# Kernel tuning notes

Measured on AMD Instinct MI355X. Metric: run time of the kernel, lower is better.

## Reference

```python
import jax, jax.numpy as jnp
import numpy as np

B, O, I, D = 8, 128, 128, 1024


def setup_inputs() -> dict:
    key = jax.random.key(0)
    ks = jax.random.split(key, 10)
    s = 1.0 / np.sqrt(2 * D)  # torch Linear default-ish scale
    return {
        "output": jax.random.normal(ks[0], (B, O, D), jnp.float32),
        "context": jax.random.normal(ks[1], (B, I, D), jnp.float32),
        "mask": jax.random.randint(ks[2], (B, I), 0, 2, jnp.int32),
        # self.w = Linear(2*dim, dim), split into the output-half and context-half
        "w_out_w": jax.random.normal(ks[3], (D, D), jnp.float32) * s,
        "w_ctx_w": jax.random.normal(ks[4], (D, D), jnp.float32) * s,
        "w_b": jax.random.normal(ks[5], (D,), jnp.float32) * s,
        # self.score = Linear(dim, 1)
        "score_w": jax.random.normal(ks[6], (D,), jnp.float32) * (1.0 / np.sqrt(D)),
        "score_b": jnp.zeros((), jnp.float32),
        # self.linear_out = Linear(2*dim, dim)
        "lin_w": jax.random.normal(ks[7], (2 * D, D), jnp.float32) * s,
        "lin_b": jax.random.normal(ks[8], (D,), jnp.float32) * s,
    }


def reference(output, context, mask, w_out_w, w_ctx_w, w_b, score_w, score_b, lin_w, lin_b):
    # Additive (Bahdanau) attention.
    # cat(out, ctx) @ W^T == out @ W1 + ctx @ W2  -> avoid [B,O,I,2D] concat.
    s_out = jnp.einsum('bod,de->boe', output, w_out_w)            # [B,O,D]
    s_ctx = jnp.einsum('bid,de->bie', context, w_ctx_w)           # [B,I,D]
    h = jax.nn.leaky_relu(s_out[:, :, None, :] + s_ctx[:, None, :, :] + w_b)  # [B,O,I,D]
    score = jnp.einsum('boid,d->boi', h, score_w) + score_b       # [B,O,I]
    score = jnp.where(mask[:, None, :] == 1, -jnp.inf, score)
    attn = jax.nn.softmax(score, axis=-1)                         # [B,O,I]
    attn_output = jnp.einsum('boi,bid->bod', attn, context)       # mix=True: bmm
    # fn=True: linear_out on cat(attn_output, output) then leaky_relu
    combined = jnp.concatenate([attn_output, output], axis=-1)    # [B,O,2D]
    attn_output = jax.nn.leaky_relu(combined @ lin_w + lin_b)     # [B,O,D]
    return attn_output, attn
```

## Files before the change

### kernel.cpp

```cpp
#include <hip/hip_runtime.h>

namespace {

constexpr int kB = 8, kO = 128, kI = 128, kD = 1024;
constexpr long kOutAttnOff = (long)kB * kO * kD;

typedef __attribute__((ext_vector_type(8))) short short8;
typedef __attribute__((ext_vector_type(4))) float f32x4;

__device__ __forceinline__ float leaky(float x) { return fmaxf(x, 0.01f * x); }

__device__ __forceinline__ short f2bf(float f) {
    unsigned u = __builtin_bit_cast(unsigned, f);
    u += 0x7FFFu + ((u >> 16) & 1u);
    return (short)(u >> 16);
}

__device__ __forceinline__ void gll16(const void* g, void* l) {
    __builtin_amdgcn_global_load_lds(
        (const __attribute__((address_space(1))) int*)g,
        (__attribute__((address_space(3))) int*)l, 16, 0, 0);
}

__global__ __launch_bounds__(256)
void conv_all(const float* __restrict__ output, const float* __restrict__ context,
              const float* __restrict__ w1, const float* __restrict__ w2,
              const float* __restrict__ lin,
              short* __restrict__ ob16, short* __restrict__ cb16,
              short* __restrict__ w1t, short* __restrict__ w2t,
              short* __restrict__ lint)
{
    __shared__ float T[64][68];
    const int bid = blockIdx.x, tid = threadIdx.x;

    if (bid < 1024) {
        const int idx = bid * 256 + tid;
        const float* src; short* dst; int i;
        if (idx < (1 << 17)) { src = output;  dst = ob16; i = idx; }
        else                 { src = context; dst = cb16; i = idx - (1 << 17); }
        const float4* s4 = (const float4*)src + (long)i * 2;
        const float4 v0 = s4[0], v1 = s4[1];
        short8 r;
        r[0] = f2bf(v0.x); r[1] = f2bf(v0.y); r[2] = f2bf(v0.z); r[3] = f2bf(v0.w);
        r[4] = f2bf(v1.x); r[5] = f2bf(v1.y); r[6] = f2bf(v1.z); r[7] = f2bf(v1.w);
        *(short8*)(dst + (long)i * 8) = r;
        return;
    }

    const int tb = bid - 1024;
    const float* src; short* dst; long C, R; int t2;
    if (tb < 256)      { src = w1;  dst = w1t;  R = 1024; C = 1024; t2 = tb; }
    else if (tb < 512) { src = w2;  dst = w2t;  R = 1024; C = 1024; t2 = tb - 256; }
    else               { src = lin; dst = lint; R = 2048; C = 1024; t2 = tb - 512; }
    const int tr = t2 >> 4, tc = t2 & 15;
    const int r = tid >> 2, q = tid & 3;

    const float* s = src + (long)(tr * 64 + r) * C + tc * 64 + q * 16;
    const float4 a0 = ((const float4*)s)[0];
    const float4 a1 = ((const float4*)s)[1];
    const float4 a2 = ((const float4*)s)[2];
    const float4 a3 = ((const float4*)s)[3];
    *(float4*)&T[r][q * 16 + 0]  = a0;
    *(float4*)&T[r][q * 16 + 4]  = a1;
    *(float4*)&T[r][q * 16 + 8]  = a2;
    *(float4*)&T[r][q * 16 + 12] = a3;
    __syncthreads();

    short8 o0, o1;
#pragma unroll
    for (int j = 0; j < 8; ++j)  o0[j] = f2bf(T[q * 16 + j][r]);
#pragma unroll
    for (int j = 0; j < 8; ++j)  o1[j] = f2bf(T[q * 16 + 8 + j][r]);
    short* dp = dst + (long)(tc * 64 + r) * R + tr * 64 + q * 16;
    *(short8*)dp       = o0;
    *((short8*)dp + 1) = o1;
}

__global__ __launch_bounds__(256)
void mm_jobs(const short* __restrict__ ob16, const short* __restrict__ cb16,
             const short* __restrict__ w1t, const short* __restrict__ w2t,
             const short* __restrict__ lint,
             const float* __restrict__ w_b, const float* __restrict__ lin_b,
             float* __restrict__ s_out, float* __restrict__ s_ctx,
             float* __restrict__ outlin, short* __restrict__ ctxlin)
{
    __shared__ short As[2][64][64];
    __shared__ short Bs[2][128][64];
    const int tid = threadIdx.x;
    const int t = blockIdx.x;
    const int lane = tid & 63, w = tid >> 6;

    const short *Ap, *Bp;
    int lda, ldb, bm, bn, ldc;
    const float* bias = nullptr;
    float* Cf = nullptr;
    short* Ch = nullptr;

    if (t < 384) {
        const int job = t >> 7, jt = t & 127;
        bm = (jt >> 3) * 64; bn = (jt & 7) * 128;
        lda = 1024; ldc = 1024;
        if (job == 0)      { Ap = ob16; Bp = w1t;         ldb = 1024; bias = w_b;   Cf = s_out;  }
        else if (job == 1) { Ap = cb16; Bp = w2t;         ldb = 1024;               Cf = s_ctx;  }
        else               { Ap = ob16; Bp = lint + 1024; ldb = 2048; bias = lin_b; Cf = outlin; }
    } else {
        const int tt = t - 384, bz = tt >> 4, tw = tt & 15;
        bm = tw * 64; bn = 0;
        Ap = lint; lda = 2048;
        Bp = cb16 + (long)bz * (kI * kD); ldb = 1024;
        Ch = ctxlin + (long)bz * (kD * kI); ldc = 128;
    }

    const int m0 = (w >> 1) * 32, n0 = (w & 1) * 64;
    const int fr = lane & 15, fcol = lane >> 4, sl = lane & 7;
    const int r8 = lane >> 3;
    const int sw8 = ((lane & 7) ^ r8) * 8;
    const int w16 = w * 16, w32 = w * 32;

    f32x4 acc[2][4] = {};

    auto stage = [&](int buf, int k0) {
        const short* ga = Ap + (long)(bm + w16 + r8) * lda + k0 + sw8;
        gll16(ga,                 &As[buf][w16][0]);
        gll16(ga + 8 * (long)lda, &As[buf][w16 + 8][0]);
        const short* gb = Bp + (long)(bn + w32 + r8) * ldb + k0 + sw8;
        gll16(gb,                  &Bs[buf][w32][0]);
        gll16(gb + 8 * (long)ldb,  &Bs[buf][w32 + 8][0]);
        gll16(gb + 16 * (long)ldb, &Bs[buf][w32 + 16][0]);
        gll16(gb + 24 * (long)ldb, &Bs[buf][w32 + 24][0]);
    };

    stage(0, 0);
    __syncthreads();
    int cur = 0;
    for (int s = 0; s < 16; ++s) {
        if (s < 15) stage(cur ^ 1, (s + 1) << 6);
#pragma unroll
        for (int ks8 = 0; ks8 < 8; ks8 += 4) {
            const int sa = ((ks8 + fcol) ^ sl) * 8;
            short8 a[2], b[4];
#pragma unroll
            for (int mi = 0; mi < 2; ++mi)
                a[mi] = *(const short8*)&As[cur][m0 + mi * 16 + fr][sa];
#pragma unroll
            for (int ni = 0; ni < 4; ++ni)
                b[ni] = *(const short8*)&Bs[cur][n0 + ni * 16 + fr][sa];
#pragma unroll
            for (int mi = 0; mi < 2; ++mi)
#pragma unroll
                for (int ni = 0; ni < 4; ++ni)
                    acc[mi][ni] = __builtin_amdgcn_mfma_f32_16x16x32_bf16(
                        a[mi], b[ni], acc[mi][ni], 0, 0, 0);
        }
        __syncthreads();
        cur ^= 1;
    }

    float bv[4] = {0, 0, 0, 0};
    if (bias) {
#pragma unroll
        for (int ni = 0; ni < 4; ++ni) bv[ni] = bias[bn + n0 + ni * 16 + fr];
    }
#pragma unroll
    for (int mi = 0; mi < 2; ++mi)
#pragma unroll
        for (int ni = 0; ni < 4; ++ni)
#pragma unroll
            for (int r = 0; r < 4; ++r) {
                const int row = bm + m0 + mi * 16 + ((lane >> 4) << 2) + r;
                const int col = bn + n0 + ni * 16 + fr;
                float v = acc[mi][ni][r] + bv[ni];
                if (Ch) Ch[(long)row * ldc + col] = f2bf(v);
                else    Cf[(long)row * ldc + col] = v;
            }
}

__global__ __launch_bounds__(256)
void score_softmax5(const float* __restrict__ s_out, const float* __restrict__ s_ctx,
                    const float* __restrict__ score_w, const float* __restrict__ score_b,
                    const int* __restrict__ mask, float* __restrict__ attn_f32,
                    short* __restrict__ attn_b16)
{
    __shared__ float As[4][1032];
    __shared__ float Cs[2][128][64];
    __shared__ float Wsh[1024];
    __shared__ float Ps[4][4][128];
    __shared__ int   Msk[128];

    const int b   = blockIdx.x;
    const int o0  = blockIdx.y * 4;
    const int tid = threadIdx.x;
    const int wv  = tid >> 6;
    const int ln  = tid & 63;

    const float* arow = s_out + (long)(b * kO + o0) * kD;
#pragma unroll
    for (int q = 0; q < 4; ++q) {
        const int tq = tid + q * 256;
        const int rr = tq >> 8, c4 = (tq & 255) * 4;
        *(float4*)&As[rr][c4] = *(const float4*)&arow[(long)rr * kD + c4];
    }
    *(float4*)&Wsh[tid * 4] = *(const float4*)&score_w[tid * 4];
    if (tid < 128) Msk[tid] = mask[b * kI + tid];

    const float* crow = s_ctx + (long)b * kI * kD;
    const int srow = wv * 4 + (ln >> 4);
    const int cho  = ((ln & 15) ^ (srow & 7)) * 4;

    auto stageCs = [&](int buf, int dc) {
#pragma unroll
        for (int it = 0; it < 8; ++it)
            gll16(crow + (long)(srow + it * 16) * kD + dc + cho,
                  &Cs[buf][wv * 4 + it * 16][0]);
    };

    float a0[4] = {}, a1[4] = {};
    const int kb = wv * 16;

    stageCs(0, 0);
    __syncthreads();
    int buf = 0;
    for (int c = 0; c < 16; ++c) {
        const int dc = c * 64;
        if (c < 15) stageCs(buf ^ 1, dc + 64);
#pragma unroll
        for (int kq = 0; kq < 4; ++kq) {
            const int sc = ((wv * 4 + kq) ^ (ln & 7)) * 4;
            const float4 c0 = *(const float4*)&Cs[buf][ln][sc];
            const float4 c1 = *(const float4*)&Cs[buf][ln + 64][sc];
            const float4 w4 = *(const float4*)&Wsh[dc + kb + kq * 4];
#pragma unroll
            for (int o = 0; o < 4; ++o) {
                const float4 av = *(const float4*)&As[o][dc + kb + kq * 4];
                a0[o] = fmaf(leaky(av.x + c0.x), w4.x, a0[o]);
                a0[o] = fmaf(leaky(av.y + c0.y), w4.y, a0[o]);
                a0[o] = fmaf(leaky(av.z + c0.z), w4.z, a0[o]);
                a0[o] = fmaf(leaky(av.w + c0.w), w4.w, a0[o]);
                a1[o] = fmaf(leaky(av.x + c1.x), w4.x, a1[o]);
                a1[o] = fmaf(leaky(av.y + c1.y), w4.y, a1[o]);
                a1[o] = fmaf(leaky(av.z + c1.z), w4.z, a1[o]);
                a1[o] = fmaf(leaky(av.w + c1.w), w4.w, a1[o]);
            }
        }
        __syncthreads();
        buf ^= 1;
    }

#pragma unroll
    for (int o = 0; o < 4; ++o) {
        Ps[wv][o][ln]      = a0[o];
        Ps[wv][o][ln + 64] = a1[o];
    }
    __syncthreads();

    const int ow = wv;
    const float negInf = -__builtin_huge_valf();
    const float sb = score_b[0];
    float s0 = Ps[0][ow][ln]      + Ps[1][ow][ln]
             + Ps[2][ow][ln]      + Ps[3][ow][ln]      + sb;
    float s1 = Ps[0][ow][ln + 64] + Ps[1][ow][ln + 64]
             + Ps[2][ow][ln + 64] + Ps[3][ow][ln + 64] + sb;
    if (Msk[ln]      != 0) s0 = negInf;
    if (Msk[ln + 64] != 0) s1 = negInf;

    float m = fmaxf(s0, s1);
#pragma unroll
    for (int d = 1; d < 64; d <<= 1) m = fmaxf(m, __shfl_xor(m, d, 64));
    const float e0 = __expf(s0 - m);
    const float e1 = __expf(s1 - m);
    float sum = e0 + e1;
#pragma unroll
    for (int d = 1; d < 64; d <<= 1) sum += __shfl_xor(sum, d, 64);
    const float inv = 1.0f / sum;

    const long rowoff = (long)(b * kO + o0 + ow) * kI;
    float* ro = attn_f32 + rowoff;
    short* rh = attn_b16 + rowoff;
    const float p0 = e0 * inv, p1 = e1 * inv;
    ro[ln]      = p0;
    ro[ln + 64] = p1;
    rh[ln]      = f2bf(p0);
    rh[ln + 64] = f2bf(p1);
}

__global__ __launch_bounds__(256)
void gemm_final(const short* __restrict__ A, const short* __restrict__ Bt,
                const float* __restrict__ addend, float* __restrict__ C)
{
    __shared__ short As[2][64][64];
    __shared__ short Bs[2][64][64];
    const int tid = threadIdx.x;
    const int bn = blockIdx.x * 64, bm = blockIdx.y * 64;
    const long z = blockIdx.z;
    const short* Az = A + z * (long)(kO * kI);
    const short* Bz = Bt + z * (long)(kD * kI);
    const float* adz = addend + z * (long)(kO * kD);
    float* Cz = C + z * (long)(kO * kD);

    const int lane = tid & 63, w = tid >> 6;
    const int w16 = w * 16;
    const int m0 = (w >> 1) * 32, n0 = (w & 1) * 32;
    const int fr = lane & 15, fcol = lane >> 4, sl = lane & 7;
    const int r8 = lane >> 3;
    const int sw8 = ((lane & 7) ^ r8) * 8;

    f32x4 acc[2][2] = {};

    auto stage = [&](int buf, int k0) {
        const short* ga = Az + (long)(bm + w16 + r8) * kI + k0 + sw8;
        gll16(ga,          &As[buf][w16][0]);
        gll16(ga + 8 * kI, &As[buf][w16 + 8][0]);
        const short* gb = Bz + (long)(bn + w16 + r8) * kI + k0 + sw8;
        gll16(gb,          &Bs[buf][w16][0]);
        gll16(gb + 8 * kI, &Bs[buf][w16 + 8][0]);
    };

    stage(0, 0);
    __syncthreads();
    int cur = 0;
    for (int s = 0; s < 2; ++s) {
        if (s == 0) stage(1, 64);
#pragma unroll
        for (int ks8 = 0; ks8 < 8; ks8 += 4) {
            const int sa = ((ks8 + fcol) ^ sl) * 8;
            const short8 a0 = *(const short8*)&As[cur][m0 + fr][sa];
            const short8 a1 = *(const short8*)&As[cur][m0 + 16 + fr][sa];
            const short8 b0 = *(const short8*)&Bs[cur][n0 + fr][sa];
            const short8 b1 = *(const short8*)&Bs[cur][n0 + 16 + fr][sa];
            acc[0][0] = __builtin_amdgcn_mfma_f32_16x16x32_bf16(a0, b0, acc[0][0], 0, 0, 0);
            acc[0][1] = __builtin_amdgcn_mfma_f32_16x16x32_bf16(a0, b1, acc[0][1], 0, 0, 0);
            acc[1][0] = __builtin_amdgcn_mfma_f32_16x16x32_bf16(a1, b0, acc[1][0], 0, 0, 0);
            acc[1][1] = __builtin_amdgcn_mfma_f32_16x16x32_bf16(a1, b1, acc[1][1], 0, 0, 0);
        }
        __syncthreads();
        cur ^= 1;
    }

#pragma unroll
    for (int mi = 0; mi < 2; ++mi)
#pragma unroll
        for (int ni = 0; ni < 2; ++ni)
#pragma unroll
            for (int r = 0; r < 4; ++r) {
                const int row = bm + m0 + mi * 16 + ((lane >> 4) << 2) + r;
                const int col = bn + n0 + ni * 16 + fr;
                const float v = acc[mi][ni][r] + adz[(long)row * kD + col];
                Cz[(long)row * kD + col] = leaky(v);
            }
}

}

extern "C" void kernel_launch(void* const* d_in, const int* in_sizes, int n_in,
                              void* d_out, int out_size, void* d_ws, size_t ws_size,
                              hipStream_t stream)
{
    const float* output  = (const float*)d_in[0];
    const float* context = (const float*)d_in[1];
    const int*   mask    = (const int*)d_in[2];
    const float* w_out_w = (const float*)d_in[3];
    const float* w_ctx_w = (const float*)d_in[4];
    const float* w_b     = (const float*)d_in[5];
    const float* score_w = (const float*)d_in[6];
    const float* score_b = (const float*)d_in[7];
    const float* lin_w   = (const float*)d_in[8];
    const float* lin_b   = (const float*)d_in[9];

    float* out_main = (float*)d_out;
    float* out_attn = out_main + kOutAttnOff;
    float* s_out    = out_main;

    char* wp = (char*)d_ws;
    float* s_ctx  = (float*)wp;  wp += (size_t)4 << 20;
    short* ob16   = (short*)wp;  wp += (size_t)2 << 20;
    short* cb16   = (short*)wp;  wp += (size_t)2 << 20;
    short* w1t    = (short*)wp;  wp += (size_t)2 << 20;
    short* w2t    = (short*)wp;  wp += (size_t)2 << 20;
    short* lint   = (short*)wp;  wp += (size_t)4 << 20;
    float* outlin = (float*)wp;  wp += (size_t)4 << 20;
    short* ctxlin = (short*)wp;  wp += (size_t)2 << 20;
    short* attn16 = (short*)wp;

    const dim3 blk(256);

    hipLaunchKernelGGL(conv_all, dim3(2048), blk, 0, stream,
        output, context, w_out_w, w_ctx_w, lin_w, ob16, cb16, w1t, w2t, lint);

    hipLaunchKernelGGL(mm_jobs, dim3(512), blk, 0, stream,
        ob16, cb16, w1t, w2t, lint, w_b, lin_b, s_out, s_ctx, outlin, ctxlin);

    hipLaunchKernelGGL(score_softmax5, dim3(8, 32), blk, 0, stream,
        s_out, s_ctx, score_w, score_b, mask, out_attn, attn16);

    hipLaunchKernelGGL(gemm_final, dim3(16, 2, 8), blk, 0, stream,
        attn16, ctxlin, outlin, out_main);
}
```

Measured before the change: 68.55 us.

## Fuse score softmax with final attention GEMM and rewrite leaky ReLU via abs

Merges the score/softmax kernel and the final attn·ctx GEMM into one kernel. Softmax probabilities stay in LDS as bf16 and feed MFMA tiles directly, which drops a launch and the bf16 attention round trip through global memory. Leaky ReLU is rewritten exactly as 0.505x + 0.495|x|. The linear part is split into a per-row output dot product and a per-column context dot product computed once, so the hot inner loop becomes add plus FMA with an abs modifier. In exchange, each block re-reads its batch's full ctxlin matrix and runs 16-row MFMAs with only 4 useful rows.

Result: slower. 72.30 us (+5.5%).

```diff
diff --git a/kernel.cpp b/kernel.cpp
--- a/kernel.cpp
+++ b/kernel.cpp
@@ -176,22 +176,28 @@
 }
 
 __global__ __launch_bounds__(256)
-void score_softmax5(const float* __restrict__ s_out, const float* __restrict__ s_ctx,
-                    const float* __restrict__ score_w, const float* __restrict__ score_b,
-                    const int* __restrict__ mask, float* __restrict__ attn_f32,
-                    short* __restrict__ attn_b16)
+void score_final(const float* __restrict__ s_out, const float* __restrict__ s_ctx,
+                 const float* __restrict__ score_w, const float* __restrict__ score_b,
+                 const int* __restrict__ mask, const short* __restrict__ ctxlin,
+                 const float* __restrict__ outlin, float* __restrict__ out_main,
+                 float* __restrict__ attn_f32)
 {
     __shared__ float As[4][1032];
-    __shared__ float Cs[2][128][64];
+    __shared__ __align__(16) char CsPool[65536];
     __shared__ float Wsh[1024];
     __shared__ float Ps[4][4][128];
+    __shared__ float Psi[4][128];
+    __shared__ float so_sh[4];
     __shared__ int   Msk[128];
-
+    __shared__ short Pl[16][136];
+
+    float (*Cs)[128][64] = reinterpret_cast<float(*)[128][64]>(CsPool);
     const int b   = blockIdx.x;
     const int o0  = blockIdx.y * 4;
     const int tid = threadIdx.x;
     const int wv  = tid >> 6;
     const int ln  = tid & 63;
+    const int fr  = ln & 15;
 
     const float* arow = s_out + (long)(b * kO + o0) * kD;
 #pragma unroll
@@ -202,6 +208,10 @@
     }
     *(float4*)&Wsh[tid * 4] = *(const float4*)&score_w[tid * 4];
     if (tid < 128) Msk[tid] = mask[b * kI + tid];
+    {
+        short* pf = &Pl[0][0];
+        for (int j = tid; j < 272; j += 256) *(short8*)(pf + j * 8) = short8{};
+    }
 
     const float* crow = s_ctx + (long)b * kI * kD;
     const int srow = wv * 4 + (ln >> 4);
@@ -214,11 +224,27 @@
                   &Cs[buf][wv * 4 + it * 16][0]);
     };
 
-    float a0[4] = {}, a1[4] = {};
-    const int kb = wv * 16;
-
     stageCs(0, 0);
     __syncthreads();
+
+    {
+        float acc = 0.0f;
+#pragma unroll
+        for (int j = 0; j < 16; j += 4) {
+            const float4 av = *(const float4*)&As[wv][ln * 16 + j];
+            const float4 ww = *(const float4*)&Wsh[ln * 16 + j];
+            acc = fmaf(av.x, ww.x, acc); acc = fmaf(av.y, ww.y, acc);
+            acc = fmaf(av.z, ww.z, acc); acc = fmaf(av.w, ww.w, acc);
+        }
+#pragma unroll
+        for (int d = 1; d < 64; d <<= 1) acc += __shfl_xor(acc, d, 64);
+        if (ln == 0) so_sh[wv] = acc;
+    }
+
+    float sa0[4] = {}, sa1[4] = {};
+    float si0 = 0.0f, si1 = 0.0f;
+    const int kb = wv * 16;
+
     int buf = 0;
     for (int c = 0; c < 16; ++c) {
         const int dc = c * 64;
@@ -229,17 +255,21 @@
             const float4 c0 = *(const float4*)&Cs[buf][ln][sc];
             const float4 c1 = *(const float4*)&Cs[buf][ln + 64][sc];
             const float4 w4 = *(const float4*)&Wsh[dc + kb + kq * 4];
+            si0 = fmaf(c0.x, w4.x, si0); si0 = fmaf(c0.y, w4.y, si0);
+            si0 = fmaf(c0.z, w4.z, si0); si0 = fmaf(c0.w, w4.w, si0);
+            si1 = fmaf(c1.x, w4.x, si1); si1 = fmaf(c1.y, w4.y, si1);
+            si1 = fmaf(c1.z, w4.z, si1); si1 = fmaf(c1.w, w4.w, si1);
 #pragma unroll
             for (int o = 0; o < 4; ++o) {
                 const float4 av = *(const float4*)&As[o][dc + kb + kq * 4];
-                a0[o] = fmaf(leaky(av.x + c0.x), w4.x, a0[o]);
-                a0[o] = fmaf(leaky(av.y + c0.y), w4.y, a0[o]);
-                a0[o] = fmaf(leaky(av.z + c0.z), w4.z, a0[o]);
-                a0[o] = fmaf(leaky(av.w + c0.w), w4.w, a0[o]);
-                a1[o] = fmaf(leaky(av.x + c1.x), w4.x, a1[o]);
-                a1[o] = fmaf(leaky(av.y + c1.y), w4.y, a1[o]);
-                a1[o] = fmaf(leaky(av.z + c1.z), w4.z, a1[o]);
-                a1[o] = fmaf(leaky(av.w + c1.w), w4.w, a1[o]);
+                sa0[o] = fmaf(__builtin_fabsf(av.x + c0.x), w4.x, sa0[o]);
+                sa0[o] = fmaf(__builtin_fabsf(av.y + c0.y), w4.y, sa0[o]);
+                sa0[o] = fmaf(__builtin_fabsf(av.z + c0.z), w4.z, sa0[o]);
+                sa0[o] = fmaf(__builtin_fabsf(av.w + c0.w), w4.w, sa0[o]);
+                sa1[o] = fmaf(__builtin_fabsf(av.x + c1.x), w4.x, sa1[o]);
+                sa1[o] = fmaf(__builtin_fabsf(av.y + c1.y), w4.y, sa1[o]);
+                sa1[o] = fmaf(__builtin_fabsf(av.z + c1.z), w4.z, sa1[o]);
+                sa1[o] = fmaf(__builtin_fabsf(av.w + c1.w), w4.w, sa1[o]);
             }
         }
         __syncthreads();
@@ -248,105 +278,95 @@
 
 #pragma unroll
     for (int o = 0; o < 4; ++o) {
-        Ps[wv][o][ln]      = a0[o];
-        Ps[wv][o][ln + 64] = a1[o];
-    }
+        Ps[wv][o][ln]      = sa0[o];
+        Ps[wv][o][ln + 64] = sa1[o];
+    }
+    Psi[wv][ln]      = si0;
+    Psi[wv][ln + 64] = si1;
     __syncthreads();
 
-    const int ow = wv;
-    const float negInf = -__builtin_huge_valf();
-    const float sb = score_b[0];
-    float s0 = Ps[0][ow][ln]      + Ps[1][ow][ln]
-             + Ps[2][ow][ln]      + Ps[3][ow][ln]      + sb;
-    float s1 = Ps[0][ow][ln + 64] + Ps[1][ow][ln + 64]
-             + Ps[2][ow][ln + 64] + Ps[3][ow][ln + 64] + sb;
-    if (Msk[ln]      != 0) s0 = negInf;
-    if (Msk[ln + 64] != 0) s1 = negInf;
-
-    float m = fmaxf(s0, s1);
-#pragma unroll
-    for (int d = 1; d < 64; d <<= 1) m = fmaxf(m, __shfl_xor(m, d, 64));
-    const float e0 = __expf(s0 - m);
-    const float e1 = __expf(s1 - m);
-    float sum = e0 + e1;
-#pragma unroll
-    for (int d = 1; d < 64; d <<= 1) sum += __shfl_xor(sum, d, 64);
-    const float inv = 1.0f / sum;
-
-    const long rowoff = (long)(b * kO + o0 + ow) * kI;
-    float* ro = attn_f32 + rowoff;
-    short* rh = attn_b16 + rowoff;
-    const float p0 = e0 * inv, p1 = e1 * inv;
-    ro[ln]      = p0;
-    ro[ln + 64] = p1;
-    rh[ln]      = f2bf(p0);
-    rh[ln + 64] = f2bf(p1);
-}
-
-__global__ __launch_bounds__(256)
-void gemm_final(const short* __restrict__ A, const short* __restrict__ Bt,
-                const float* __restrict__ addend, float* __restrict__ C)
-{
-    __shared__ short As[2][64][64];
-    __shared__ short Bs[2][64][64];
-    const int tid = threadIdx.x;
-    const int bn = blockIdx.x * 64, bm = blockIdx.y * 64;
-    const long z = blockIdx.z;
-    const short* Az = A + z * (long)(kO * kI);
-    const short* Bz = Bt + z * (long)(kD * kI);
-    const float* adz = addend + z * (long)(kO * kD);
-    float* Cz = C + z * (long)(kO * kD);
-
-    const int lane = tid & 63, w = tid >> 6;
-    const int w16 = w * 16;
-    const int m0 = (w >> 1) * 32, n0 = (w & 1) * 32;
-    const int fr = lane & 15, fcol = lane >> 4, sl = lane & 7;
-    const int r8 = lane >> 3;
-    const int sw8 = ((lane & 7) ^ r8) * 8;
-
-    f32x4 acc[2][2] = {};
-
-    auto stage = [&](int buf, int k0) {
-        const short* ga = Az + (long)(bm + w16 + r8) * kI + k0 + sw8;
-        gll16(ga,          &As[buf][w16][0]);
-        gll16(ga + 8 * kI, &As[buf][w16 + 8][0]);
-        const short* gb = Bz + (long)(bn + w16 + r8) * kI + k0 + sw8;
-        gll16(gb,          &Bs[buf][w16][0]);
-        gll16(gb + 8 * kI, &Bs[buf][w16 + 8][0]);
+    {
+        const int ow = wv;
+        const float negInf = -__builtin_huge_valf();
+        const float sb = score_b[0];
+        const float siT0 = Psi[0][ln] + Psi[1][ln] + Psi[2][ln] + Psi[3][ln];
+        const float siT1 = Psi[0][ln + 64] + Psi[1][ln + 64]
+                         + Psi[2][ln + 64] + Psi[3][ln + 64];
+        const float saT0 = Ps[0][ow][ln] + Ps[1][ow][ln]
+                         + Ps[2][ow][ln] + Ps[3][ow][ln];
+        const float saT1 = Ps[0][ow][ln + 64] + Ps[1][ow][ln + 64]
+                         + Ps[2][ow][ln + 64] + Ps[3][ow][ln + 64];
+        const float soV = so_sh[ow];
+        float s0 = 0.505f * (soV + siT0) + 0.495f * saT0 + sb;
+        float s1 = 0.505f * (soV + siT1) + 0.495f * saT1 + sb;
+        if (Msk[ln]      != 0) s0 = negInf;
+        if (Msk[ln + 64] != 0) s1 = negInf;
+
+        float m = fmaxf(s0, s1);
+#pragma unroll
+        for (int d = 1; d < 64; d <<= 1) m = fmaxf(m, __shfl_xor(m, d, 64));
+        const float e0 = __expf(s0 - m);
+        const float e1 = __expf(s1 - m);
+        float sum = e0 + e1;
+#pragma unroll
+        for (int d = 1; d < 64; d <<= 1) sum += __shfl_xor(sum, d, 64);
+        const float inv = 1.0f / sum;
+
+        const long rowoff = (long)(b * kO + o0 + ow) * kI;
+        const float p0 = e0 * inv, p1 = e1 * inv;
+        attn_f32[rowoff + ln]      = p0;
+        attn_f32[rowoff + ln + 64] = p1;
+        Pl[ow][ln]      = f2bf(p0);
+        Pl[ow][ln + 64] = f2bf(p1);
+    }
+
+    short* Bsh = (short*)CsPool;
+    const short* ctxb = ctxlin + (long)b * (kD * kI);
+    auto stageB = [&](int half, int nc) {
+        short* dst = Bsh + half * (128 * 128);
+#pragma unroll
+        for (int it = 0; it < 8; ++it) {
+            const int rb = wv * 32 + it * 4;
+            const int r  = rb + (ln >> 4);
+            const int gn = nc * 128 + r;
+            const int sc = (ln & 15) ^ (r & 7);
+            gll16(ctxb + (long)gn * kI + sc * 8, dst + rb * 128);
+        }
     };
 
-    stage(0, 0);
+    stageB(0, 0);
     __syncthreads();
-    int cur = 0;
-    for (int s = 0; s < 2; ++s) {
-        if (s == 0) stage(1, 64);
-#pragma unroll
-        for (int ks8 = 0; ks8 < 8; ks8 += 4) {
-            const int sa = ((ks8 + fcol) ^ sl) * 8;
-            const short8 a0 = *(const short8*)&As[cur][m0 + fr][sa];
-            const short8 a1 = *(const short8*)&As[cur][m0 + 16 + fr][sa];
-            const short8 b0 = *(const short8*)&Bs[cur][n0 + fr][sa];
-            const short8 b1 = *(const short8*)&Bs[cur][n0 + 16 + fr][sa];
-            acc[0][0] = __builtin_amdgcn_mfma_f32_16x16x32_bf16(a0, b0, acc[0][0], 0, 0, 0);
-            acc[0][1] = __builtin_amdgcn_mfma_f32_16x16x32_bf16(a0, b1, acc[0][1], 0, 0, 0);
-            acc[1][0] = __builtin_amdgcn_mfma_f32_16x16x32_bf16(a1, b0, acc[1][0], 0, 0, 0);
-            acc[1][1] = __builtin_amdgcn_mfma_f32_16x16x32_bf16(a1, b1, acc[1][1], 0, 0, 0);
+    int half = 0;
+    const int fg = ln >> 4;
+    for (int nc = 0; nc < 8; ++nc) {
+        if (nc < 7) stageB(half ^ 1, nc + 1);
+        const short* Bc = Bsh + half * (128 * 128);
+        f32x4 accT0{}, accT1{};
+#pragma unroll
+        for (int ks = 0; ks < 4; ++ks) {
+            const short8 a = *(const short8*)&Pl[fr][ks * 32 + fg * 8];
+            const int n0 = (wv * 2) * 16 + fr;
+            const int n1 = (wv * 2 + 1) * 16 + fr;
+            const int ch0 = ((ks * 4 + fg) ^ (n0 & 7)) * 8;
+            const int ch1 = ((ks * 4 + fg) ^ (n1 & 7)) * 8;
+            const short8 b0 = *(const short8*)&Bc[n0 * 128 + ch0];
+            const short8 b1 = *(const short8*)&Bc[n1 * 128 + ch1];
+            accT0 = __builtin_amdgcn_mfma_f32_16x16x32_bf16(a, b0, accT0, 0, 0, 0);
+            accT1 = __builtin_amdgcn_mfma_f32_16x16x32_bf16(a, b1, accT1, 0, 0, 0);
+        }
+        if (fg == 0) {
+#pragma unroll
+            for (int r = 0; r < 4; ++r) {
+                const long off = (long)(b * kO + o0 + r) * kD;
+                const int na = nc * 128 + (wv * 2) * 16 + fr;
+                const int nb = nc * 128 + (wv * 2 + 1) * 16 + fr;
+                out_main[off + na] = leaky(accT0[r] + outlin[off + na]);
+                out_main[off + nb] = leaky(accT1[r] + outlin[off + nb]);
+            }
         }
         __syncthreads();
-        cur ^= 1;
-    }
-
-#pragma unroll
-    for (int mi = 0; mi < 2; ++mi)
-#pragma unroll
-        for (int ni = 0; ni < 2; ++ni)
-#pragma unroll
-            for (int r = 0; r < 4; ++r) {
-                const int row = bm + m0 + mi * 16 + ((lane >> 4) << 2) + r;
-                const int col = bn + n0 + ni * 16 + fr;
-                const float v = acc[mi][ni][r] + adz[(long)row * kD + col];
-                Cz[(long)row * kD + col] = leaky(v);
-            }
+        half ^= 1;
+    }
 }
 
 }
@@ -379,7 +399,6 @@
     short* lint   = (short*)wp;  wp += (size_t)4 << 20;
     float* outlin = (float*)wp;  wp += (size_t)4 << 20;
     short* ctxlin = (short*)wp;  wp += (size_t)2 << 20;
-    short* attn16 = (short*)wp;
 
     const dim3 blk(256);
 
@@ -389,9 +408,6 @@
     hipLaunchKernelGGL(mm_jobs, dim3(512), blk, 0, stream,
         ob16, cb16, w1t, w2t, lint, w_b, lin_b, s_out, s_ctx, outlin, ctxlin);
 
-    hipLaunchKernelGGL(score_softmax5, dim3(8, 32), blk, 0, stream,
-        s_out, s_ctx, score_w, score_b, mask, out_attn, attn16);
-
-    hipLaunchKernelGGL(gemm_final, dim3(16, 2, 8), blk, 0, stream,
-        attn16, ctxlin, outlin, out_main);
-}
+    hipLaunchKernelGGL(score_final, dim3(8, 32), blk, 0, stream,
+        s_out, s_ctx, score_w, score_b, mask, ctxlin, outlin, out_main, out_attn);
+}
```
